# Optimization experiments

Hardware: AMD Instinct MI355X
Metric: run time of the kernel (lower is better)

Reference implementation:

```python
import jax, jax.numpy as jnp
import numpy as np
from jax import lax

NUM_CLASSES = 5
N_ITER = 3
IC = 32 * 14 * 14  # 6272 primary capsules
IN_DIM = 14
OUT_DIM = 1


def squash(s):
    # s: [B, N, D]; squash along capsule dim D (dim=2 in torch code)
    sq = jnp.sum(s * s, axis=2)
    scale = sq / (1.0 + sq) / jnp.sqrt(sq)
    return s * scale[:, :, None]


def setup_inputs() -> dict:
    key = jax.random.key(0)
    ks = jax.random.split(key, 7)
    B = 1024
    inp = jax.random.normal(ks[0], (B, 1, 59, 59), dtype=jnp.float32)
    # conv1: Conv2d(1, 32, k=5, s=2)
    W1 = jax.random.normal(ks[1], (32, 1, 5, 5), dtype=jnp.float32) * 0.1
    b1 = jax.random.normal(ks[2], (32,), dtype=jnp.float32) * 0.01
    # primary caps conv: Conv2d(32, 32*14, k=1, s=2) -> 1x1 kernel stored as [448,32]
    Wp = jax.random.normal(ks[3], (32 * 14, 32), dtype=jnp.float32) * 0.1
    bp = jax.random.normal(ks[4], (32 * 14,), dtype=jnp.float32) * 0.01
    # digit caps transform weights: [input_caps, input_dim, output_caps*output_dim]
    stdv = 1.0 / np.sqrt(IC)
    caps_W = jax.random.uniform(ks[5], (IC, IN_DIM, NUM_CLASSES * OUT_DIM), dtype=jnp.float32,
                                minval=-stdv, maxval=stdv)
    # routing logits (learned, initialized zero in torch)
    b_route = jnp.zeros((IC, NUM_CLASSES), dtype=jnp.float32)
    return {"input": inp, "r": 3, "W1": W1, "b1": b1, "Wp": Wp, "bp": bp,
            "caps_W": caps_W, "b_route": b_route}


def _forward(inp, W1, b1, Wp, bp, caps_W, b_route):
    B = inp.shape[0]
    # conv1 + relu: [B,32,28,28]
    x = lax.conv_general_dilated(inp, W1, window_strides=(2, 2), padding="VALID",
                                 dimension_numbers=("NCHW", "OIHW", "NCHW"))
    x = jax.nn.relu(x + b1[None, :, None, None])
    # primary caps: 1x1 conv with stride 2 == strided slice + channel matmul
    xs = x[:, :, ::2, ::2]  # [B,32,14,14]
    pc = jnp.einsum("oc,bchw->bohw", Wp, xs) + bp[None, :, None, None]  # [B,448,14,14]
    pc = pc.reshape(B, 32, 14, 14, 14)          # [B, caps, dim, H, W]
    pc = jnp.transpose(pc, (0, 1, 3, 4, 2))     # [B, caps, H, W, dim]
    pc = pc.reshape(B, IC, IN_DIM)              # [B, 6272, 14]
    pc = squash(pc)
    # digit caps predictions: u_predict [B, IC, OC, OD]
    u = jnp.einsum("bni,nio->bno", pc, caps_W).reshape(B, IC, NUM_CLASSES, OUT_DIM)
    # routing by agreement
    c = jax.nn.softmax(b_route, axis=1)                     # [IC, OC]
    s = jnp.einsum("io,biod->bod", c, u)                    # [B, OC, OD]
    v = squash(s)
    b_batch = jnp.broadcast_to(b_route, (B, IC, NUM_CLASSES))
    for _ in range(N_ITER):
        b_batch = b_batch + jnp.sum(u * v[:, None, :, :], axis=-1)
        c = jax.nn.softmax(b_batch, axis=2)                 # [B, IC, OC]
        s = jnp.einsum("bio,biod->bod", c, u)
        v = squash(s)
    # class probabilities = capsule lengths: [B, OC]
    return jnp.sqrt(jnp.sum(v * v, axis=2))


def reference(input, r, W1, b1, Wp, bp, caps_W, b_route):
    # r is accepted but unused, matching the torch forward signature
    return _forward(input, W1, b1, Wp, bp, caps_W, b_route)
```

## Files before the change

### kernel.cpp

```cpp
#include <hip/hip_runtime.h>
#include <math.h>


#define NTH    512
#define NWAVES 8
#define IC     6272
#define NCLS   5

__global__ __launch_bounds__(NTH, 1)
void caps_fused(const float* __restrict__ inp,
                const float* __restrict__ W1,
                const float* __restrict__ b1,
                const float* __restrict__ Wp,
                const float* __restrict__ bp,
                const float* __restrict__ capsW,
                const float* __restrict__ broute,
                float* __restrict__ out)
{
    extern __shared__ float lds[];
    float* s_xs  = lds;
    float* s_W1  = s_xs + 6272;
    float* s_b1  = s_W1 + 800;
    float* s_red = s_b1 + 32;
    float* s_v   = s_red + 40;
    float* s_u   = s_v + 8;
    float* s_in  = s_u;

    const int b    = blockIdx.x;
    const int tid  = threadIdx.x;
    const int lane = tid & 63;
    const int wv   = tid >> 6;
    const int wvs  = __builtin_amdgcn_readfirstlane(wv);

    const float* inb = inp + (size_t)b * (59 * 59);
    for (int i = tid; i < 59 * 59; i += NTH) s_in[i] = inb[i];
    for (int i = tid; i < 800;     i += NTH) s_W1[i] = W1[i];
    if (tid < 32) s_b1[tid] = b1[tid];
    __syncthreads();

    for (int n = tid; n < IC; n += NTH) {
        const int c  = n / 196;
        const int hw = n - c * 196;
        const int h  = hw / 14;
        const int w  = hw - h * 14;
        const float* ip = s_in + (4 * h) * 59 + 4 * w;
        const float* wk = s_W1 + c * 25;
        float acc = s_b1[c];
        #pragma unroll
        for (int kh = 0; kh < 5; ++kh)
            #pragma unroll
            for (int kw = 0; kw < 5; ++kw)
                acc = fmaf(ip[kh * 59 + kw], wk[kh * 5 + kw], acc);
        const int col = 4 * ((c >> 2) ^ (hw & 7)) + (c & 3);
        s_xs[hw * 32 + col] = fmaxf(acc, 0.0f);
    }
    __syncthreads();

    const float4* xs4 = (const float4*)s_xs;

    #define EMIT(PC, HW)                                                    \
    {                                                                       \
        if ((HW) < 196) {                                                   \
            const int n = g * 196 + (HW);                                   \
            float sq = 0.f;                                                 \
            _Pragma("unroll")                                               \
            for (int i = 0; i < 14; ++i) sq = fmaf(PC[i], PC[i], sq);       \
            const float scale = sqrtf(sq) / (1.0f + sq);                    \
            float uo[NCLS] = {0.f, 0.f, 0.f, 0.f, 0.f};                     \
            const float* cw = capsW + (size_t)n * 70;                       \
            _Pragma("unroll")                                               \
            for (int i = 0; i < 14; ++i) {                                  \
                const float p = PC[i] * scale;                              \
                _Pragma("unroll")                                           \
                for (int o = 0; o < NCLS; ++o)                              \
                    uo[o] = fmaf(p, cw[i * 5 + o], uo[o]);                  \
            }                                                               \
            _Pragma("unroll")                                               \
            for (int o = 0; o < NCLS; ++o) s_u[n * 5 + o] = uo[o];          \
        }                                                                   \
    }

    for (int gi = 0; gi < 4; ++gi) {
        const int g = wvs + gi * 8;
        const float* wpg = Wp + g * 448;
        const float* bpg = bp + g * 14;

        #pragma unroll
        for (int p = 0; p < 2; ++p) {
            const int hwA = p * 128 + lane;
            const int hwB = p ? (192 + (lane & 3)) : (64 + lane);
            float xA[32], xB[32];
            #pragma unroll
            for (int j = 0; j < 8; ++j) {
                const float4 a  = xs4[hwA * 8 + (j ^ (hwA & 7))];
                const float4 bb = xs4[hwB * 8 + (j ^ (hwB & 7))];
                xA[4*j+0] = a.x;  xA[4*j+1] = a.y;  xA[4*j+2] = a.z;  xA[4*j+3] = a.w;
                xB[4*j+0] = bb.x; xB[4*j+1] = bb.y; xB[4*j+2] = bb.z; xB[4*j+3] = bb.w;
            }

            float pcA[14], pcB[14];
            #pragma unroll
            for (int i = 0; i < 14; ++i) {
                const float bias = bpg[i];
                pcA[i] = bias; pcB[i] = bias;
            }
            #pragma unroll
            for (int i = 0; i < 14; ++i) {
                const float* wr = wpg + i * 32;
                #pragma unroll
                for (int c = 0; c < 32; ++c) {
                    const float w = wr[c];
                    pcA[i] = fmaf(w, xA[c], pcA[i]);
                    pcB[i] = fmaf(w, xB[c], pcB[i]);
                }
            }
            EMIT(pcA, hwA)
            EMIT(pcB, hwB)
        }
    }
    #undef EMIT
    __syncthreads();

    float V[NCLS] = {0.f, 0.f, 0.f, 0.f, 0.f};
    for (int it = 0; it < 4; ++it) {
        float sacc[NCLS] = {0.f, 0.f, 0.f, 0.f, 0.f};
        for (int n = tid; n < IC; n += NTH) {
            const float* br = broute + (size_t)n * 5;
            float uu[NCLS], l[NCLS];
            #pragma unroll
            for (int o = 0; o < NCLS; ++o) {
                uu[o] = s_u[n * 5 + o];
                l[o]  = fmaf(uu[o], V[o], br[o]);
            }
            const float m = fmaxf(fmaxf(fmaxf(l[0], l[1]), fmaxf(l[2], l[3])), l[4]);
            float e[NCLS], es = 0.f;
            #pragma unroll
            for (int o = 0; o < NCLS; ++o) { e[o] = __expf(l[o] - m); es += e[o]; }
            const float inv = 1.0f / es;
            #pragma unroll
            for (int o = 0; o < NCLS; ++o)
                sacc[o] = fmaf(uu[o], e[o] * inv, sacc[o]);
        }
        #pragma unroll
        for (int off = 32; off > 0; off >>= 1)
            #pragma unroll
            for (int o = 0; o < NCLS; ++o)
                sacc[o] += __shfl_down(sacc[o], off);
        if (lane == 0) {
            #pragma unroll
            for (int o = 0; o < NCLS; ++o) s_red[wv * 5 + o] = sacc[o];
        }
        __syncthreads();
        if (tid == 0) {
            #pragma unroll
            for (int o = 0; o < NCLS; ++o) {
                float s = 0.f;
                for (int w2 = 0; w2 < NWAVES; ++w2) s += s_red[w2 * 5 + o];
                s_v[o] = s * fabsf(s) / (1.0f + s * s);
            }
        }
        __syncthreads();
        #pragma unroll
        for (int o = 0; o < NCLS; ++o) V[o] += s_v[o];
    }

    if (tid < NCLS) out[b * NCLS + tid] = fabsf(s_v[tid]);
}

extern "C" void kernel_launch(void* const* d_in, const int* in_sizes, int n_in,
                              void* d_out, int out_size, void* d_ws, size_t ws_size,
                              hipStream_t stream)
{
    const float* inp   = (const float*)d_in[0];
    const float* W1    = (const float*)d_in[2];
    const float* b1    = (const float*)d_in[3];
    const float* Wp    = (const float*)d_in[4];
    const float* bp    = (const float*)d_in[5];
    const float* capsW = (const float*)d_in[6];
    const float* brt   = (const float*)d_in[7];
    float* out = (float*)d_out;

    const int B = in_sizes[0] / (59 * 59);
    const size_t lds_bytes = (size_t)(6272 + 800 + 32 + 40 + 8 + 31360) * sizeof(float);
    (void)hipFuncSetAttribute((const void*)caps_fused,
                              hipFuncAttributeMaxDynamicSharedMemorySize,
                              (int)lds_bytes);
    caps_fused<<<B, NTH, lds_bytes, stream>>>(inp, W1, b1, Wp, bp, capsW, brt, out);
}
```

Baseline: 686.9 us.

## Split fused capsule kernel into prediction and routing kernels via workspace

```diff
diff --git a/kernel.cpp b/kernel.cpp
--- a/kernel.cpp
+++ b/kernel.cpp
@@ -6,6 +6,161 @@
 #define NWAVES 8
 #define IC     6272
 #define NCLS   5
+
+__global__ __launch_bounds__(NTH, 1)
+void caps_u(const float* __restrict__ inp,
+            const float* __restrict__ W1,
+            const float* __restrict__ b1,
+            const float* __restrict__ Wp,
+            const float* __restrict__ bp,
+            const float* __restrict__ capsW,
+            float* __restrict__ uws)
+{
+    extern __shared__ float lds[];
+    float* s_in  = lds;
+    float* s_W1  = s_in + 3481;
+    float* s_b1  = s_W1 + 800;
+    float* s_xs  = s_b1 + 32;
+
+    const int b    = blockIdx.x;
+    const int tid  = threadIdx.x;
+    const int lane = tid & 63;
+    const int wv   = tid >> 6;
+    const int wvs  = __builtin_amdgcn_readfirstlane(wv);
+
+    const float* inb = inp + (size_t)b * (59 * 59);
+    for (int i = tid; i < 59 * 59; i += NTH) s_in[i] = inb[i];
+    for (int i = tid; i < 800;     i += NTH) s_W1[i] = W1[i];
+    if (tid < 32) s_b1[tid] = b1[tid];
+    __syncthreads();
+
+    for (int n = tid; n < IC; n += NTH) {
+        const int c  = n / 196;
+        const int hw = n - c * 196;
+        const int h  = hw / 14;
+        const int w  = hw - h * 14;
+        const float* ip = s_in + (4 * h) * 59 + 4 * w;
+        const float* wk = s_W1 + c * 25;
+        float acc = s_b1[c];
+        #pragma unroll
+        for (int kh = 0; kh < 5; ++kh)
+            #pragma unroll
+            for (int kw = 0; kw < 5; ++kw)
+                acc = fmaf(ip[kh * 59 + kw], wk[kh * 5 + kw], acc);
+        const int col = 4 * ((c >> 2) ^ (hw & 7)) + (c & 3);
+        s_xs[hw * 32 + col] = fmaxf(acc, 0.0f);
+    }
+    __syncthreads();
+
+    const float4* xs4 = (const float4*)s_xs;
+    float* ub = uws + (size_t)b * 5 * IC;
+
+    for (int gi = 0; gi < 4; ++gi) {
+        const int g = wvs + gi * 8;
+        const float* wpg = Wp + g * 448;
+        const float* bpg = bp + g * 14;
+
+        #pragma unroll
+        for (int r = 0; r < 4; ++r) {
+            const int hw = (r < 3) ? (r * 64 + lane) : (192 + (lane & 3));
+            float x[32];
+            #pragma unroll
+            for (int j = 0; j < 8; ++j) {
+                const float4 a = xs4[hw * 8 + (j ^ (hw & 7))];
+                x[4*j+0] = a.x; x[4*j+1] = a.y; x[4*j+2] = a.z; x[4*j+3] = a.w;
+            }
+            float pc[14];
+            #pragma unroll
+            for (int i = 0; i < 14; ++i) pc[i] = bpg[i];
+            #pragma unroll
+            for (int i = 0; i < 14; ++i) {
+                const float* wr = wpg + i * 32;
+                #pragma unroll
+                for (int c = 0; c < 32; ++c)
+                    pc[i] = fmaf(wr[c], x[c], pc[i]);
+            }
+            if (r < 3 || lane < 4) {
+                const int n = g * 196 + hw;
+                float sq = 0.f;
+                #pragma unroll
+                for (int i = 0; i < 14; ++i) sq = fmaf(pc[i], pc[i], sq);
+                const float scale = sqrtf(sq) / (1.0f + sq);
+                float uo[NCLS] = {0.f, 0.f, 0.f, 0.f, 0.f};
+                const float* cw = capsW + (size_t)n * 70;
+                #pragma unroll
+                for (int i = 0; i < 14; ++i) {
+                    const float p = pc[i] * scale;
+                    #pragma unroll
+                    for (int o = 0; o < NCLS; ++o)
+                        uo[o] = fmaf(p, cw[i * 5 + o], uo[o]);
+                }
+                #pragma unroll
+                for (int o = 0; o < NCLS; ++o) ub[o * IC + n] = uo[o];
+            }
+        }
+    }
+}
+
+__global__ __launch_bounds__(NTH, 1)
+void caps_route(const float* __restrict__ uws,
+                const float* __restrict__ broute,
+                float* __restrict__ out)
+{
+    __shared__ float s_red[NWAVES * NCLS];
+    __shared__ float s_v[8];
+
+    const int b    = blockIdx.x;
+    const int tid  = threadIdx.x;
+    const int lane = tid & 63;
+    const int wv   = tid >> 6;
+
+    const float* ub = uws + (size_t)b * 5 * IC;
+
+    float V[NCLS] = {0.f, 0.f, 0.f, 0.f, 0.f};
+    for (int it = 0; it < 4; ++it) {
+        float sacc[NCLS] = {0.f, 0.f, 0.f, 0.f, 0.f};
+        for (int n = tid; n < IC; n += NTH) {
+            const float* br = broute + (size_t)n * 5;
+            float uu[NCLS], l[NCLS];
+            #pragma unroll
+            for (int o = 0; o < NCLS; ++o) {
+                uu[o] = ub[o * IC + n];
+                l[o]  = fmaf(uu[o], V[o], br[o]);
+            }
+            const float m = fmaxf(fmaxf(fmaxf(l[0], l[1]), fmaxf(l[2], l[3])), l[4]);
+            float e[NCLS], es = 0.f;
+            #pragma unroll
+            for (int o = 0; o < NCLS; ++o) { e[o] = __expf(l[o] - m); es += e[o]; }
+            const float inv = 1.0f / es;
+            #pragma unroll
+            for (int o = 0; o < NCLS; ++o)
+                sacc[o] = fmaf(uu[o], e[o] * inv, sacc[o]);
+        }
+        #pragma unroll
+        for (int off = 32; off > 0; off >>= 1)
+            #pragma unroll
+            for (int o = 0; o < NCLS; ++o)
+                sacc[o] += __shfl_down(sacc[o], off);
+        if (lane == 0) {
+            #pragma unroll
+            for (int o = 0; o < NCLS; ++o) s_red[wv * 5 + o] = sacc[o];
+        }
+        __syncthreads();
+        if (tid == 0) {
+            #pragma unroll
+            for (int o = 0; o < NCLS; ++o) {
+                float s = 0.f;
+                for (int w2 = 0; w2 < NWAVES; ++w2) s += s_red[w2 * 5 + o];
+                s_v[o] = s * fabsf(s) / (1.0f + s * s);
+            }
+        }
+        __syncthreads();
+        #pragma unroll
+        for (int o = 0; o < NCLS; ++o) V[o] += s_v[o];
+    }
+
+    if (tid < NCLS) out[b * NCLS + tid] = fabsf(s_v[tid]);
+}
 
 __global__ __launch_bounds__(NTH, 1)
 void caps_fused(const float* __restrict__ inp,
@@ -57,68 +212,49 @@
     __syncthreads();
 
     const float4* xs4 = (const float4*)s_xs;
-
-    #define EMIT(PC, HW)                                                    \
-    {                                                                       \
-        if ((HW) < 196) {                                                   \
-            const int n = g * 196 + (HW);                                   \
-            float sq = 0.f;                                                 \
-            _Pragma("unroll")                                               \
-            for (int i = 0; i < 14; ++i) sq = fmaf(PC[i], PC[i], sq);       \
-            const float scale = sqrtf(sq) / (1.0f + sq);                    \
-            float uo[NCLS] = {0.f, 0.f, 0.f, 0.f, 0.f};                     \
-            const float* cw = capsW + (size_t)n * 70;                       \
-            _Pragma("unroll")                                               \
-            for (int i = 0; i < 14; ++i) {                                  \
-                const float p = PC[i] * scale;                              \
-                _Pragma("unroll")                                           \
-                for (int o = 0; o < NCLS; ++o)                              \
-                    uo[o] = fmaf(p, cw[i * 5 + o], uo[o]);                  \
-            }                                                               \
-            _Pragma("unroll")                                               \
-            for (int o = 0; o < NCLS; ++o) s_u[n * 5 + o] = uo[o];          \
-        }                                                                   \
-    }
-
     for (int gi = 0; gi < 4; ++gi) {
         const int g = wvs + gi * 8;
         const float* wpg = Wp + g * 448;
         const float* bpg = bp + g * 14;
-
-        #pragma unroll
-        for (int p = 0; p < 2; ++p) {
-            const int hwA = p * 128 + lane;
-            const int hwB = p ? (192 + (lane & 3)) : (64 + lane);
-            float xA[32], xB[32];
+        #pragma unroll
+        for (int r = 0; r < 4; ++r) {
+            const int hw = (r < 3) ? (r * 64 + lane) : (192 + (lane & 3));
+            float x[32];
             #pragma unroll
             for (int j = 0; j < 8; ++j) {
-                const float4 a  = xs4[hwA * 8 + (j ^ (hwA & 7))];
-                const float4 bb = xs4[hwB * 8 + (j ^ (hwB & 7))];
-                xA[4*j+0] = a.x;  xA[4*j+1] = a.y;  xA[4*j+2] = a.z;  xA[4*j+3] = a.w;
-                xB[4*j+0] = bb.x; xB[4*j+1] = bb.y; xB[4*j+2] = bb.z; xB[4*j+3] = bb.w;
-            }
-
-            float pcA[14], pcB[14];
-            #pragma unroll
-            for (int i = 0; i < 14; ++i) {
-                const float bias = bpg[i];
-                pcA[i] = bias; pcB[i] = bias;
-            }
+                const float4 a = xs4[hw * 8 + (j ^ (hw & 7))];
+                x[4*j+0] = a.x; x[4*j+1] = a.y; x[4*j+2] = a.z; x[4*j+3] = a.w;
+            }
+            float pc[14];
+            #pragma unroll
+            for (int i = 0; i < 14; ++i) pc[i] = bpg[i];
             #pragma unroll
             for (int i = 0; i < 14; ++i) {
                 const float* wr = wpg + i * 32;
                 #pragma unroll
-                for (int c = 0; c < 32; ++c) {
-                    const float w = wr[c];
-                    pcA[i] = fmaf(w, xA[c], pcA[i]);
-                    pcB[i] = fmaf(w, xB[c], pcB[i]);
+                for (int c = 0; c < 32; ++c)
+                    pc[i] = fmaf(wr[c], x[c], pc[i]);
+            }
+            if (r < 3 || lane < 4) {
+                const int n = g * 196 + hw;
+                float sq = 0.f;
+                #pragma unroll
+                for (int i = 0; i < 14; ++i) sq = fmaf(pc[i], pc[i], sq);
+                const float scale = sqrtf(sq) / (1.0f + sq);
+                float uo[NCLS] = {0.f, 0.f, 0.f, 0.f, 0.f};
+                const float* cw = capsW + (size_t)n * 70;
+                #pragma unroll
+                for (int i = 0; i < 14; ++i) {
+                    const float p = pc[i] * scale;
+                    #pragma unroll
+                    for (int o = 0; o < NCLS; ++o)
+                        uo[o] = fmaf(p, cw[i * 5 + o], uo[o]);
                 }
-            }
-            EMIT(pcA, hwA)
-            EMIT(pcB, hwB)
-        }
-    }
-    #undef EMIT
+                #pragma unroll
+                for (int o = 0; o < NCLS; ++o) s_u[n * 5 + o] = uo[o];
+            }
+        }
+    }
     __syncthreads();
 
     float V[NCLS] = {0.f, 0.f, 0.f, 0.f, 0.f};
@@ -181,9 +317,17 @@
     float* out = (float*)d_out;
 
     const int B = in_sizes[0] / (59 * 59);
-    const size_t lds_bytes = (size_t)(6272 + 800 + 32 + 40 + 8 + 31360) * sizeof(float);
-    (void)hipFuncSetAttribute((const void*)caps_fused,
-                              hipFuncAttributeMaxDynamicSharedMemorySize,
-                              (int)lds_bytes);
-    caps_fused<<<B, NTH, lds_bytes, stream>>>(inp, W1, b1, Wp, bp, capsW, brt, out);
+    const size_t ws_need = (size_t)B * 5 * IC * sizeof(float);
+
+    if (ws_size >= ws_need) {
+        const size_t lds1 = (size_t)(3481 + 800 + 32 + 6272) * sizeof(float);
+        caps_u<<<B, NTH, lds1, stream>>>(inp, W1, b1, Wp, bp, capsW, (float*)d_ws);
+        caps_route<<<B, NTH, 0, stream>>>((const float*)d_ws, brt, out);
+    } else {
+        const size_t lds_bytes = (size_t)(6272 + 800 + 32 + 40 + 8 + 31360) * sizeof(float);
+        (void)hipFuncSetAttribute((const void*)caps_fused,
+                                  hipFuncAttributeMaxDynamicSharedMemorySize,
+                                  (int)lds_bytes);
+        caps_fused<<<B, NTH, lds_bytes, stream>>>(inp, W1, b1, Wp, bp, capsW, brt, out);
+    }
 }
```

Result: slower. 1.058 ms (+54.0%).
